# Kernel tuning notes

Hardware: AMD Instinct MI355X
Metric: run time of the kernel (lower is better)

## Reference

```python
import jax, jax.numpy as jnp
import numpy as np

N = 100000
E = 1600000
H = 64      # hidden_size
NH = 8      # num_heads
DH = H // NH  # per-head dim (heads are the LAST axis, as in the torch code)


def _lin(x, W, b):
    return x @ W + b


def setup_inputs() -> dict:
    key = jax.random.key(0)
    ks = jax.random.split(key, 18)
    s = 0.05
    inp = {
        "h_x": jax.random.normal(ks[0], (N, H), jnp.float32),
        "h_e": jax.random.normal(ks[1], (E, H), jnp.float32),
        "row": jax.random.randint(ks[2], (E,), 0, N, jnp.int32),  # dst node of each nonzero
        "col": jax.random.randint(ks[3], (E,), 0, N, jnp.int32),  # src node of each nonzero
    }
    names = ["q", "k", "v", "e", "oh", "oe"]
    for i, nm in enumerate(names):
        inp["W" + nm] = jax.random.normal(ks[4 + 2 * i], (H, H), jnp.float32) * s
        inp["b" + nm] = jax.random.normal(ks[5 + 2 * i], (H,), jnp.float32) * s
    return inp


def reference(h_x, h_e, row, col, Wq, bq, Wk, bk, Wv, bv, We, be, Woh, boh, Woe, boe):
    n = h_x.shape[0]
    m = h_e.shape[0]
    q = _lin(h_x, Wq, bq).reshape(n, DH, NH)
    k = _lin(h_x, Wk, bk).reshape(n, DH, NH)
    v = _lin(h_x, Wv, bv).reshape(n, DH, NH)
    e = _lin(h_e, We, be).reshape(m, DH, NH)

    # SDDMM: per-nonzero (i=row, j=col), per-head dot of q[i] and k[j]  -> (E, NH)
    scores = (q[row] * k[col]).sum(axis=1) / jnp.sqrt(jnp.float32(DH))

    # edge gating: e.sum over dh axis -> (E, NH)
    e_gate = e.sum(axis=1)
    scores = scores * e_gate

    # oe branch (uses pre-softmax gated scores)
    oe_feat = scores[:, None, :] * e          # (E, DH, NH)
    oe = _lin(oe_feat.reshape(m, H), Woe, boe)

    # sparse softmax over dim=1 (per destination row), per head
    mx = jax.ops.segment_max(scores, row, num_segments=n)      # (N, NH)
    ex = jnp.exp(scores - mx[row])
    den = jax.ops.segment_sum(ex, row, num_segments=n)         # (N, NH)
    sm = ex / den[row]                                          # (E, NH)

    # bSpMM: h_out[i,:,h] = sum_{e: row[e]=i} sm[e,h] * v[col[e],:,h]
    h_out = jax.ops.segment_sum(sm[:, None, :] * v[col], row, num_segments=n)
    oh = _lin(h_out.reshape(n, H), Woh, boh)
    return (oh, oe)
```

## Files before the change

### kernel.cpp

```cpp
#include <hip/hip_runtime.h>

typedef __attribute__((ext_vector_type(8))) short bf16x8;
typedef __attribute__((ext_vector_type(4))) float f32x4;

__device__ __forceinline__ unsigned short f2bf(float f) {
  unsigned u = __float_as_uint(f);
  return (unsigned short)((u + 0x7fffu + ((u >> 16) & 1u)) >> 16);
}
__device__ __forceinline__ float bf2f(unsigned short h) {
  return __uint_as_float(((unsigned)h) << 16);
}

template<bool IN_BF16, bool OUT_BF16>
__global__ void __launch_bounds__(256) gemm64_kernel(const void* __restrict__ Ain,
    const float* __restrict__ W, const float* __restrict__ bias,
    void* __restrict__ Out, int M) {
  const int tid = threadIdx.x;
  const int l = tid & 63;
  const int g = l >> 4;
  const int n15 = l & 15;

  bf16x8 bfrag[4][2];
  float bv[4];
#pragma unroll
  for (int nb = 0; nb < 4; ++nb) {
    bv[nb] = bias[nb * 16 + n15];
#pragma unroll
    for (int kb = 0; kb < 2; ++kb)
#pragma unroll
      for (int j = 0; j < 8; ++j)
        bfrag[nb][kb][j] = (short)f2bf(W[(kb * 32 + g * 8 + j) * 64 + nb * 16 + n15]);
  }

  int wid = (blockIdx.x * blockDim.x + tid) >> 6;
  int nw = (gridDim.x * blockDim.x) >> 6;
  int ntiles = (M + 15) >> 4;
  for (int t = wid; t < ntiles; t += nw) {
    int m0 = t << 4;
    int arow = m0 + n15;
    bf16x8 a0, a1;
    if (arow < M) {
      if constexpr (IN_BF16) {
        const unsigned short* ap = (const unsigned short*)Ain + (size_t)arow * 64 + g * 8;
        a0 = *(const bf16x8*)ap;
        a1 = *(const bf16x8*)(ap + 32);
      } else {
        const float* ap = (const float*)Ain + (size_t)arow * 64 + g * 8;
        f32x4 x0 = *(const f32x4*)ap, x1 = *(const f32x4*)(ap + 4);
        f32x4 x2 = *(const f32x4*)(ap + 32), x3 = *(const f32x4*)(ap + 36);
#pragma unroll
        for (int j = 0; j < 4; ++j) {
          a0[j] = (short)f2bf(x0[j]); a0[4 + j] = (short)f2bf(x1[j]);
          a1[j] = (short)f2bf(x2[j]); a1[4 + j] = (short)f2bf(x3[j]);
        }
      }
    } else {
#pragma unroll
      for (int j = 0; j < 8; ++j) { a0[j] = 0; a1[j] = 0; }
    }
    f32x4 acc[4];
#pragma unroll
    for (int nb = 0; nb < 4; ++nb) {
      acc[nb] = (f32x4){bv[nb], bv[nb], bv[nb], bv[nb]};
      acc[nb] = __builtin_amdgcn_mfma_f32_16x16x32_bf16(a0, bfrag[nb][0], acc[nb], 0, 0, 0);
      acc[nb] = __builtin_amdgcn_mfma_f32_16x16x32_bf16(a1, bfrag[nb][1], acc[nb], 0, 0, 0);
    }
#pragma unroll
    for (int nb = 0; nb < 4; ++nb)
#pragma unroll
      for (int r = 0; r < 4; ++r) {
        int orow = m0 + g * 4 + r;
        if (orow < M) {
          float val = acc[nb][r];
          size_t oidx = (size_t)orow * 64 + nb * 16 + n15;
          if constexpr (OUT_BF16) ((unsigned short*)Out)[oidx] = f2bf(val);
          else                    ((float*)Out)[oidx] = val;
        }
      }
  }
}

__global__ void __launch_bounds__(256) qkv3_kernel(const float* __restrict__ hx,
    const float* __restrict__ Wq, const float* __restrict__ bq,
    const float* __restrict__ Wk, const float* __restrict__ bk,
    const float* __restrict__ Wv, const float* __restrict__ bv,
    unsigned short* __restrict__ q, unsigned short* __restrict__ k,
    unsigned short* __restrict__ v, int M) {
  const int tid = threadIdx.x;
  const int l = tid & 63;
  const int g = l >> 4;
  const int n15 = l & 15;
  const float* Ws[3] = {Wq, Wk, Wv};
  const float* bs[3] = {bq, bk, bv};
  unsigned short* outs[3] = {q, k, v};

  bf16x8 bfrag[3][4][2];
  float bvv[3][4];
#pragma unroll
  for (int w = 0; w < 3; ++w)
#pragma unroll
    for (int nb = 0; nb < 4; ++nb) {
      bvv[w][nb] = bs[w][nb * 16 + n15];
#pragma unroll
      for (int kb = 0; kb < 2; ++kb)
#pragma unroll
        for (int j = 0; j < 8; ++j)
          bfrag[w][nb][kb][j] = (short)f2bf(Ws[w][(kb * 32 + g * 8 + j) * 64 + nb * 16 + n15]);
    }

  int wid = (blockIdx.x * blockDim.x + tid) >> 6;
  int nw = (gridDim.x * blockDim.x) >> 6;
  int ntiles = (M + 15) >> 4;
  for (int t = wid; t < ntiles; t += nw) {
    int m0 = t << 4;
    int arow = m0 + n15;
    bf16x8 a0, a1;
    if (arow < M) {
      const float* ap = hx + (size_t)arow * 64 + g * 8;
      f32x4 x0 = *(const f32x4*)ap, x1 = *(const f32x4*)(ap + 4);
      f32x4 x2 = *(const f32x4*)(ap + 32), x3 = *(const f32x4*)(ap + 36);
#pragma unroll
      for (int j = 0; j < 4; ++j) {
        a0[j] = (short)f2bf(x0[j]); a0[4 + j] = (short)f2bf(x1[j]);
        a1[j] = (short)f2bf(x2[j]); a1[4 + j] = (short)f2bf(x3[j]);
      }
    } else {
#pragma unroll
      for (int j = 0; j < 8; ++j) { a0[j] = 0; a1[j] = 0; }
    }
#pragma unroll
    for (int w = 0; w < 3; ++w) {
      f32x4 acc[4];
#pragma unroll
      for (int nb = 0; nb < 4; ++nb) {
        acc[nb] = (f32x4){bvv[w][nb], bvv[w][nb], bvv[w][nb], bvv[w][nb]};
        acc[nb] = __builtin_amdgcn_mfma_f32_16x16x32_bf16(a0, bfrag[w][nb][0], acc[nb], 0, 0, 0);
        acc[nb] = __builtin_amdgcn_mfma_f32_16x16x32_bf16(a1, bfrag[w][nb][1], acc[nb], 0, 0, 0);
      }
#pragma unroll
      for (int nb = 0; nb < 4; ++nb)
#pragma unroll
        for (int r = 0; r < 4; ++r) {
          int orow = m0 + g * 4 + r;
          if (orow < M)
            outs[w][(size_t)orow * 64 + nb * 16 + n15] = f2bf(acc[nb][r]);
        }
    }
  }
}

__global__ void __launch_bounds__(256, 3) edge_fused_kernel(
    const float* __restrict__ he,
    const int* __restrict__ rowi, const int* __restrict__ coli,
    const unsigned short* __restrict__ qb, const unsigned short* __restrict__ kbuf,
    const float* __restrict__ We, const float* __restrict__ be,
    const float* __restrict__ Woe, const float* __restrict__ boe,
    float* __restrict__ oe, float* __restrict__ scores,
    int* __restrict__ deg, int E) {
  const int tid = threadIdx.x;
  const int wv = tid >> 6;
  const int l = tid & 63;
  const int g = l >> 4;
  const int n15 = l & 15;
  const int h = n15 & 7;

  __shared__ float s_lds[4][160];
  __shared__ unsigned short feat_lds[4][16 * 72];

  bf16x8 bfE[4][2], bfO[4][2];
  float beV[4], boV[4];
#pragma unroll
  for (int nb = 0; nb < 4; ++nb) {
    beV[nb] = be[nb * 16 + n15];
    boV[nb] = boe[nb * 16 + n15];
#pragma unroll
    for (int kb = 0; kb < 2; ++kb)
#pragma unroll
      for (int j = 0; j < 8; ++j) {
        bfE[nb][kb][j] = (short)f2bf(We[(kb * 32 + g * 8 + j) * 64 + nb * 16 + n15]);
        bfO[nb][kb][j] = (short)f2bf(Woe[(kb * 32 + g * 8 + j) * 64 + nb * 16 + n15]);
      }
  }

  const int ntiles = (E + 15) >> 4;
  const int nit = (ntiles + 3) >> 2;
  for (int it = blockIdx.x; it < nit; it += gridDim.x) {
    const int m0 = ((it << 2) + wv) << 4;
    const int arow = m0 + n15;
    bf16x8 a0, a1;
    if (arow < E) {
      const float* ap = he + (size_t)arow * 64 + g * 8;
      f32x4 x0 = *(const f32x4*)ap, x1 = *(const f32x4*)(ap + 4);
      f32x4 x2 = *(const f32x4*)(ap + 32), x3 = *(const f32x4*)(ap + 36);
#pragma unroll
      for (int j = 0; j < 4; ++j) {
        a0[j] = (short)f2bf(x0[j]); a0[4 + j] = (short)f2bf(x1[j]);
        a1[j] = (short)f2bf(x2[j]); a1[4 + j] = (short)f2bf(x3[j]);
      }
    } else {
#pragma unroll
      for (int j = 0; j < 8; ++j) { a0[j] = 0; a1[j] = 0; }
    }
    f32x4 acc[4];
#pragma unroll
    for (int nb = 0; nb < 4; ++nb) {
      acc[nb] = (f32x4){beV[nb], beV[nb], beV[nb], beV[nb]};
      acc[nb] = __builtin_amdgcn_mfma_f32_16x16x32_bf16(a0, bfE[nb][0], acc[nb], 0, 0, 0);
      acc[nb] = __builtin_amdgcn_mfma_f32_16x16x32_bf16(a1, bfE[nb][1], acc[nb], 0, 0, 0);
    }
    float gc[4];
#pragma unroll
    for (int r = 0; r < 4; ++r) {
      float s = acc[0][r] + acc[1][r] + acc[2][r] + acc[3][r];
      s += __shfl_xor(s, 8, 64);
      gc[r] = s * 0.35355339059327373f;
    }
    const int esafe = (arow < E) ? arow : (E - 1);
    const int rq = rowi[esafe], rc = coli[esafe];
    if (g == 0 && arow < E) atomicAdd(&deg[rq], 1);
    const unsigned short* qp = qb + (size_t)rq * 64 + g * 16;
    const unsigned short* kp = kbuf + (size_t)rc * 64 + g * 16;
    bf16x8 qv0 = *(const bf16x8*)qp, qv1 = *(const bf16x8*)(qp + 8);
    bf16x8 kv0 = *(const bf16x8*)kp, kv1 = *(const bf16x8*)(kp + 8);
    float p[8];
#pragma unroll
    for (int j = 0; j < 8; ++j)
      p[j] = bf2f((unsigned short)qv0[j]) * bf2f((unsigned short)kv0[j])
           + bf2f((unsigned short)qv1[j]) * bf2f((unsigned short)kv1[j]);
#pragma unroll
    for (int j = 0; j < 8; ++j) {
      p[j] += __shfl_xor(p[j], 16, 64);
      p[j] += __shfl_xor(p[j], 32, 64);
    }
    if (l < 16) {
      float2* sp = (float2*)&s_lds[wv][n15 * 10];
#pragma unroll
      for (int j = 0; j < 4; ++j) sp[j] = make_float2(p[2 * j], p[2 * j + 1]);
    }
    __syncthreads();
    float srow[4];
#pragma unroll
    for (int r = 0; r < 4; ++r)
      srow[r] = s_lds[wv][(g * 4 + r) * 10 + h] * gc[r];
#pragma unroll
    for (int r = 0; r < 4; ++r) {
      int orow = m0 + g * 4 + r;
      if (n15 < 8 && orow < E) scores[(size_t)orow * 8 + n15] = srow[r];
    }
#pragma unroll
    for (int nb = 0; nb < 4; ++nb)
#pragma unroll
      for (int r = 0; r < 4; ++r)
        feat_lds[wv][(g * 4 + r) * 72 + nb * 16 + n15] = f2bf(srow[r] * acc[nb][r]);
    __syncthreads();
    const unsigned short* fpt = &feat_lds[wv][n15 * 72 + g * 8];
    a0 = *(const bf16x8*)fpt;
    a1 = *(const bf16x8*)(fpt + 32);
#pragma unroll
    for (int nb = 0; nb < 4; ++nb) {
      f32x4 a2 = (f32x4){boV[nb], boV[nb], boV[nb], boV[nb]};
      a2 = __builtin_amdgcn_mfma_f32_16x16x32_bf16(a0, bfO[nb][0], a2, 0, 0, 0);
      a2 = __builtin_amdgcn_mfma_f32_16x16x32_bf16(a1, bfO[nb][1], a2, 0, 0, 0);
#pragma unroll
      for (int r = 0; r < 4; ++r) {
        int orow = m0 + g * 4 + r;
        if (orow < E) oe[(size_t)orow * 64 + nb * 16 + n15] = a2[r];
      }
    }
  }
}

__global__ void zero_kernel(int* __restrict__ p, int n) {
  int i = blockIdx.x * blockDim.x + threadIdx.x;
  if (i < n) p[i] = 0;
}

#define SCAN_B 256
#define SCAN_E 8
__global__ void scan1_kernel(const int* __restrict__ deg, int* __restrict__ rowptr,
                             int* __restrict__ blksum, int n) {
  __shared__ int sh[SCAN_B];
  int base = blockIdx.x * (SCAN_B * SCAN_E) + threadIdx.x * SCAN_E;
  int v[SCAN_E];
  int s = 0;
#pragma unroll
  for (int j = 0; j < SCAN_E; ++j) {
    v[j] = (base + j < n) ? deg[base + j] : 0;
    s += v[j];
  }
  sh[threadIdx.x] = s;
  __syncthreads();
  for (int off = 1; off < SCAN_B; off <<= 1) {
    int t = (threadIdx.x >= off) ? sh[threadIdx.x - off] : 0;
    __syncthreads();
    sh[threadIdx.x] += t;
    __syncthreads();
  }
  if (threadIdx.x == SCAN_B - 1) blksum[blockIdx.x] = sh[SCAN_B - 1];
  int run = sh[threadIdx.x] - s;
#pragma unroll
  for (int j = 0; j < SCAN_E; ++j) {
    if (base + j < n) rowptr[base + j] = run;
    run += v[j];
  }
}

__global__ void scan2_kernel(int* __restrict__ blksum, int nb) {
  __shared__ int sh[SCAN_B];
  int v = (threadIdx.x < nb) ? blksum[threadIdx.x] : 0;
  sh[threadIdx.x] = v;
  __syncthreads();
  for (int off = 1; off < SCAN_B; off <<= 1) {
    int t = (threadIdx.x >= off) ? sh[threadIdx.x - off] : 0;
    __syncthreads();
    sh[threadIdx.x] += t;
    __syncthreads();
  }
  if (threadIdx.x < nb) blksum[threadIdx.x] = sh[threadIdx.x] - v;
}

__global__ void scan3_kernel(int* __restrict__ rowptr, int* __restrict__ cursor,
                             const int* __restrict__ blksum, int n) {
  int i = blockIdx.x * blockDim.x + threadIdx.x;
  if (i >= n) return;
  int v = rowptr[i] + blksum[i / (SCAN_B * SCAN_E)];
  rowptr[i] = v;
  cursor[i] = v;
}

__global__ void scatter_kernel(const int* __restrict__ row, const int* __restrict__ col,
                               int* __restrict__ cursor, int* __restrict__ eidx,
                               int* __restrict__ ecol, int E) {
  int gid = blockIdx.x * blockDim.x + threadIdx.x;
  if (gid >= E) return;
  int r = row[gid];
  int slot = atomicAdd(&cursor[r], 1);
  eidx[slot] = gid;
  ecol[slot] = col[gid];
}

__global__ void __launch_bounds__(256) row_attn_kernel(const float* __restrict__ scores,
    const int* __restrict__ rowptr, const int* __restrict__ deg,
    const int* __restrict__ eidx, const int* __restrict__ ecol,
    const unsigned short* __restrict__ vb, float* __restrict__ hout, int n) {
  int gid = blockIdx.x * blockDim.x + threadIdx.x;
  int r = gid >> 6, lane = threadIdx.x & 63;
  if (r >= n) return;
  int start = rowptr[r], dg = deg[r];
  int h = lane & 7;
  float m = -3.4e38f, den = 0.f, acc = 0.f;
  for (int i = 0; i < dg; ++i) {
    int eid = eidx[start + i];
    int c = ecol[start + i];
    float s = scores[(size_t)eid * 8 + h];
    float vv = bf2f(vb[(size_t)c * 64 + lane]);
    float mn = fmaxf(m, s);
    float corr = __expf(m - mn);
    float ex = __expf(s - mn);
    den = den * corr + ex;
    acc = acc * corr + ex * vv;
    m = mn;
  }
  hout[(size_t)r * 64 + lane] = (dg > 0) ? acc / den : 0.f;
}

extern "C" void kernel_launch(void* const* d_in, const int* in_sizes, int n_in,
                              void* d_out, int out_size, void* d_ws, size_t ws_size,
                              hipStream_t stream) {
  const float* hx  = (const float*)d_in[0];
  const float* he  = (const float*)d_in[1];
  const int*   row = (const int*)d_in[2];
  const int*   col = (const int*)d_in[3];
  const float* Wq = (const float*)d_in[4],  *bq = (const float*)d_in[5];
  const float* Wk = (const float*)d_in[6],  *bk = (const float*)d_in[7];
  const float* Wv = (const float*)d_in[8],  *bv = (const float*)d_in[9];
  const float* We = (const float*)d_in[10], *be = (const float*)d_in[11];
  const float* Woh = (const float*)d_in[12], *boh = (const float*)d_in[13];
  const float* Woe = (const float*)d_in[14], *boe = (const float*)d_in[15];

  const int n = in_sizes[0] / 64;
  const int E = in_sizes[2];

  float* out = (float*)d_out;
  float* oh = out;
  float* oe = out + (size_t)n * 64;

  unsigned short* qb   = (unsigned short*)d_ws;
  unsigned short* kb   = qb + (size_t)n * 64;
  unsigned short* vbuf = kb + (size_t)n * 64;
  float* scores = (float*)(vbuf + (size_t)n * 64);
  float* hout   = scores + (size_t)E * 8;

  int* deg    = (int*)(hout + (size_t)n * 64);
  int* rowptr = deg + n;
  int* cursor = rowptr + n;
  int* blksum = cursor + n;
  int* eidx   = blksum + 256;
  int* ecol   = eidx + (size_t)E;

  const int nb_scan = (n + SCAN_B * SCAN_E - 1) / (SCAN_B * SCAN_E);

  zero_kernel<<<(n + 255) / 256, 256, 0, stream>>>(deg, n);
  qkv3_kernel<<<512, 256, 0, stream>>>(hx, Wq, bq, Wk, bk, Wv, bv, qb, kb, vbuf, n);
  edge_fused_kernel<<<2048, 256, 0, stream>>>(he, row, col, qb, kb, We, be, Woe, boe,
                                              oe, scores, deg, E);

  scan1_kernel<<<nb_scan, SCAN_B, 0, stream>>>(deg, rowptr, blksum, n);
  scan2_kernel<<<1, SCAN_B, 0, stream>>>(blksum, nb_scan);
  scan3_kernel<<<(n + 255) / 256, 256, 0, stream>>>(rowptr, cursor, blksum, n);
  scatter_kernel<<<(E + 255) / 256, 256, 0, stream>>>(row, col, cursor, eidx, ecol, E);

  row_attn_kernel<<<(n + 3) / 4, 256, 0, stream>>>(scores, rowptr, deg, eidx, ecol,
                                                   vbuf, hout, n);
  gemm64_kernel<false, false><<<512, 256, 0, stream>>>(hout, Woh, boh, oh, n);
}
```

Before: 598.5 us.

## Build CSR before edge kernel and write scores directly in row-sorted order

Result: faster. 568.0 us (-5.1%).

```diff
diff --git a/kernel.cpp b/kernel.cpp
--- a/kernel.cpp
+++ b/kernel.cpp
@@ -9,6 +9,11 @@
 }
 __device__ __forceinline__ float bf2f(unsigned short h) {
   return __uint_as_float(((unsigned)h) << 16);
+}
+
+__device__ __forceinline__ void lds_fence() {
+  asm volatile("s_waitcnt lgkmcnt(0)" ::: "memory");
+  __builtin_amdgcn_sched_barrier(0);
 }
 
 template<bool IN_BF16, bool OUT_BF16>
@@ -149,14 +154,14 @@
   }
 }
 
-__global__ void __launch_bounds__(256, 3) edge_fused_kernel(
+__global__ void __launch_bounds__(256) edge_fused_kernel(
     const float* __restrict__ he,
     const int* __restrict__ rowi, const int* __restrict__ coli,
+    const int* __restrict__ eslot,
     const unsigned short* __restrict__ qb, const unsigned short* __restrict__ kbuf,
     const float* __restrict__ We, const float* __restrict__ be,
     const float* __restrict__ Woe, const float* __restrict__ boe,
-    float* __restrict__ oe, float* __restrict__ scores,
-    int* __restrict__ deg, int E) {
+    float* __restrict__ oe, float* __restrict__ escores, int E) {
   const int tid = threadIdx.x;
   const int wv = tid >> 6;
   const int l = tid & 63;
@@ -217,7 +222,7 @@
     }
     const int esafe = (arow < E) ? arow : (E - 1);
     const int rq = rowi[esafe], rc = coli[esafe];
-    if (g == 0 && arow < E) atomicAdd(&deg[rq], 1);
+    const int slotv = eslot[esafe];
     const unsigned short* qp = qb + (size_t)rq * 64 + g * 16;
     const unsigned short* kp = kbuf + (size_t)rc * 64 + g * 16;
     bf16x8 qv0 = *(const bf16x8*)qp, qv1 = *(const bf16x8*)(qp + 8);
@@ -237,7 +242,7 @@
 #pragma unroll
       for (int j = 0; j < 4; ++j) sp[j] = make_float2(p[2 * j], p[2 * j + 1]);
     }
-    __syncthreads();
+    lds_fence();
     float srow[4];
 #pragma unroll
     for (int r = 0; r < 4; ++r)
@@ -245,14 +250,15 @@
 #pragma unroll
     for (int r = 0; r < 4; ++r) {
       int orow = m0 + g * 4 + r;
-      if (n15 < 8 && orow < E) scores[(size_t)orow * 8 + n15] = srow[r];
+      int slot = __shfl(slotv, g * 4 + r, 64);
+      if (n15 < 8 && orow < E) escores[(size_t)slot * 8 + n15] = srow[r];
     }
 #pragma unroll
     for (int nb = 0; nb < 4; ++nb)
 #pragma unroll
       for (int r = 0; r < 4; ++r)
         feat_lds[wv][(g * 4 + r) * 72 + nb * 16 + n15] = f2bf(srow[r] * acc[nb][r]);
-    __syncthreads();
+    lds_fence();
     const unsigned short* fpt = &feat_lds[wv][n15 * 72 + g * 8];
     a0 = *(const bf16x8*)fpt;
     a1 = *(const bf16x8*)(fpt + 32);
@@ -273,6 +279,11 @@
 __global__ void zero_kernel(int* __restrict__ p, int n) {
   int i = blockIdx.x * blockDim.x + threadIdx.x;
   if (i < n) p[i] = 0;
+}
+
+__global__ void hist_kernel(const int* __restrict__ row, int* __restrict__ deg, int E) {
+  int gid = blockIdx.x * blockDim.x + threadIdx.x;
+  if (gid < E) atomicAdd(&deg[row[gid]], 1);
 }
 
 #define SCAN_B 256
@@ -329,37 +340,33 @@
 }
 
 __global__ void scatter_kernel(const int* __restrict__ row, const int* __restrict__ col,
-                               int* __restrict__ cursor, int* __restrict__ eidx,
+                               int* __restrict__ cursor, int* __restrict__ eslot,
                                int* __restrict__ ecol, int E) {
   int gid = blockIdx.x * blockDim.x + threadIdx.x;
   if (gid >= E) return;
   int r = row[gid];
   int slot = atomicAdd(&cursor[r], 1);
-  eidx[slot] = gid;
+  eslot[gid] = slot;
   ecol[slot] = col[gid];
 }
 
-__global__ void __launch_bounds__(256) row_attn_kernel(const float* __restrict__ scores,
+__global__ void __launch_bounds__(256) row_attn_kernel(const float* __restrict__ escores,
     const int* __restrict__ rowptr, const int* __restrict__ deg,
-    const int* __restrict__ eidx, const int* __restrict__ ecol,
+    const int* __restrict__ ecol,
     const unsigned short* __restrict__ vb, float* __restrict__ hout, int n) {
   int gid = blockIdx.x * blockDim.x + threadIdx.x;
   int r = gid >> 6, lane = threadIdx.x & 63;
   if (r >= n) return;
   int start = rowptr[r], dg = deg[r];
   int h = lane & 7;
-  float m = -3.4e38f, den = 0.f, acc = 0.f;
+  float den = 0.f, acc = 0.f;
+#pragma unroll 4
   for (int i = 0; i < dg; ++i) {
-    int eid = eidx[start + i];
     int c = ecol[start + i];
-    float s = scores[(size_t)eid * 8 + h];
+    float ex = __expf(escores[(size_t)(start + i) * 8 + h]);
     float vv = bf2f(vb[(size_t)c * 64 + lane]);
-    float mn = fmaxf(m, s);
-    float corr = __expf(m - mn);
-    float ex = __expf(s - mn);
-    den = den * corr + ex;
-    acc = acc * corr + ex * vv;
-    m = mn;
+    den += ex;
+    acc += ex * vv;
   }
   hout[(size_t)r * 64 + lane] = (dg > 0) ? acc / den : 0.f;
 }
@@ -388,29 +395,30 @@
   unsigned short* qb   = (unsigned short*)d_ws;
   unsigned short* kb   = qb + (size_t)n * 64;
   unsigned short* vbuf = kb + (size_t)n * 64;
-  float* scores = (float*)(vbuf + (size_t)n * 64);
-  float* hout   = scores + (size_t)E * 8;
+  float* escores = (float*)(vbuf + (size_t)n * 64);
+  float* hout    = escores + (size_t)E * 8;
 
   int* deg    = (int*)(hout + (size_t)n * 64);
   int* rowptr = deg + n;
   int* cursor = rowptr + n;
   int* blksum = cursor + n;
-  int* eidx   = blksum + 256;
-  int* ecol   = eidx + (size_t)E;
+  int* eslot  = blksum + 256;
+  int* ecol   = eslot + (size_t)E;
 
   const int nb_scan = (n + SCAN_B * SCAN_E - 1) / (SCAN_B * SCAN_E);
 
   zero_kernel<<<(n + 255) / 256, 256, 0, stream>>>(deg, n);
-  qkv3_kernel<<<512, 256, 0, stream>>>(hx, Wq, bq, Wk, bk, Wv, bv, qb, kb, vbuf, n);
-  edge_fused_kernel<<<2048, 256, 0, stream>>>(he, row, col, qb, kb, We, be, Woe, boe,
-                                              oe, scores, deg, E);
-
+  hist_kernel<<<(E + 255) / 256, 256, 0, stream>>>(row, deg, E);
   scan1_kernel<<<nb_scan, SCAN_B, 0, stream>>>(deg, rowptr, blksum, n);
   scan2_kernel<<<1, SCAN_B, 0, stream>>>(blksum, nb_scan);
   scan3_kernel<<<(n + 255) / 256, 256, 0, stream>>>(rowptr, cursor, blksum, n);
-  scatter_kernel<<<(E + 255) / 256, 256, 0, stream>>>(row, col, cursor, eidx, ecol, E);
-
-  row_attn_kernel<<<(n + 3) / 4, 256, 0, stream>>>(scores, rowptr, deg, eidx, ecol,
+  scatter_kernel<<<(E + 255) / 256, 256, 0, stream>>>(row, col, cursor, eslot, ecol, E);
+
+  qkv3_kernel<<<512, 256, 0, stream>>>(hx, Wq, bq, Wk, bk, Wv, bv, qb, kb, vbuf, n);
+  edge_fused_kernel<<<2048, 256, 0, stream>>>(he, row, col, eslot, qb, kb, We, be,
+                                              Woe, boe, oe, escores, E);
+
+  row_attn_kernel<<<(n + 3) / 4, 256, 0, stream>>>(escores, rowptr, deg, ecol,
                                                    vbuf, hout, n);
   gemm64_kernel<false, false><<<512, 256, 0, stream>>>(hout, Woh, boh, oh, n);
 }
```
